# Kernel optimization log

Hardware: AMD Instinct MI355X
Metric: run time of the kernel (lower is better)

The kernel has to match this reference:

```python
import jax, jax.numpy as jnp
import numpy as np

B, S, HIDDEN = 2, 2048, 2048
HQ, HKV, D = 16, 4, 128
EPS = 1e-6
SCALE = D ** -0.5


def _deinterleave(x):
    # [..., D] interleaved pairs -> [x0,x2,...,x1,x3,...] (half layout)
    *lead, d = x.shape
    return x.reshape(*lead, d // 2, 2).swapaxes(-1, -2).reshape(*lead, d)


def _interleave(x):
    # inverse of _deinterleave
    *lead, d = x.shape
    return x.reshape(*lead, 2, d // 2).swapaxes(-1, -2).reshape(*lead, d)


def _rotate_half(x):
    x1, x2 = jnp.split(x, 2, axis=-1)
    return jnp.concatenate([-x2, x1], axis=-1)


def _rmsnorm(x, w):
    var = jnp.mean(jnp.square(x), axis=-1, keepdims=True)
    return x * jax.lax.rsqrt(var + EPS) * w


def setup_inputs() -> dict:
    key = jax.random.key(0)
    k0, k1, k2, k3, k4 = jax.random.split(key, 5)
    hidden_states = jax.random.normal(k0, (B, S, HIDDEN), jnp.float32)
    cos = jax.random.uniform(k1, (S, D), jnp.float32, -1.0, 1.0)
    sin = jax.random.uniform(k2, (S, D), jnp.float32, -1.0, 1.0)
    qkv_w = jax.random.normal(k3, ((HQ + 2 * HKV) * D, HIDDEN), jnp.float32) * 0.02
    qk_norm_w = jnp.ones((D,), jnp.float32)
    o_w = jax.random.normal(k4, (HIDDEN, HQ * D), jnp.float32) * 0.02
    return {"hidden_states": hidden_states, "cos": cos, "sin": sin,
            "qkv_w": qkv_w, "qk_norm_w": qk_norm_w, "o_w": o_w}


def reference(hidden_states, cos, sin, qkv_w, qk_norm_w, o_w):
    b, s, _ = hidden_states.shape
    qkv = jnp.einsum('bsh,oh->bso', hidden_states, qkv_w)  # [B,S,(HQ+2HKV)*D]
    q = qkv[..., : HQ * D].reshape(b, s, HQ, D)
    k = qkv[..., HQ * D:(HQ + HKV) * D].reshape(b, s, HKV, D)
    v = qkv[..., (HQ + HKV) * D:].reshape(b, s, HKV, D)

    # interleaved-layout RoPE: deinterleave -> rotate-half RoPE -> re-interleave
    q, k = _deinterleave(q), _deinterleave(k)
    cs = cos[None, :, None, :]
    sn = sin[None, :, None, :]
    q = q * cs + _rotate_half(q) * sn
    k = k * cs + _rotate_half(k) * sn
    q, k = _interleave(q), _interleave(k)

    # QK RMSNorm (shared weight over head_dim)
    q = _rmsnorm(q, qk_norm_w)
    k = _rmsnorm(k, qk_norm_w)

    # causal GQA attention
    g = HQ // HKV
    qg = q.reshape(b, s, HKV, g, D)
    scores = jnp.einsum('bshgd,bthd->bhgst', qg, k) * SCALE  # [B,HKV,g,S,S]
    causal = jnp.tril(jnp.ones((s, s), bool))
    scores = jnp.where(causal, scores, jnp.finfo(scores.dtype).min)
    probs = jax.nn.softmax(scores, axis=-1)
    attn = jnp.einsum('bhgst,bthd->bshgd', probs, v).reshape(b, s, HQ * D)

    return jnp.einsum('bsd,od->bso', attn, o_w)
```

## Files before the change

kernel.cpp:

```cpp
#include <hip/hip_runtime.h>
#include <hip/hip_bf16.h>

typedef __bf16 bf16_t;
typedef bf16_t bf16x8 __attribute__((ext_vector_type(8)));
typedef float f32x4 __attribute__((ext_vector_type(4)));
typedef float f32x16 __attribute__((ext_vector_type(16)));
typedef unsigned short u16;
typedef unsigned int u32;

#define B_    2
#define S_    2048
#define HID   2048
#define NQKV  3072
#define HQ_   16
#define HKV_  4
#define D_    128
#define QSCALE_ 0.12751879526600565f

__device__ __forceinline__ u16 f2b(float f) {
    __hip_bfloat16 h = __float2bfloat16(f);
    return *reinterpret_cast<u16*>(&h);
}
__device__ __forceinline__ float b2f(u32 u) {
    u32 v = u << 16;
    float f;
    __builtin_memcpy(&f, &v, 4);
    return f;
}

__global__ __launch_bounds__(256) void cvt3_f32_bf16(const float* __restrict__ i0, u16* __restrict__ o0, int n0,
                                                     const float* __restrict__ i1, u16* __restrict__ o1, int n1,
                                                     const float* __restrict__ i2, u16* __restrict__ o2, int n2) {
    int i = blockIdx.x * 256 + threadIdx.x;
    const float* src; u16* dst; int idx;
    if (i < n0)           { src = i0; dst = o0; idx = i; }
    else if (i < n0 + n1) { src = i1; dst = o1; idx = i - n0; }
    else if (i < n0 + n1 + n2) { src = i2; dst = o2; idx = i - n0 - n1; }
    else return;
    float4 v = reinterpret_cast<const float4*>(src)[idx];
    ushort4 o;
    o.x = f2b(v.x); o.y = f2b(v.y); o.z = f2b(v.z); o.w = f2b(v.w);
    reinterpret_cast<ushort4*>(dst)[idx] = o;
}

template<bool BF16OUT>
__global__ __launch_bounds__(256, 2) void gemm128sq(const u16* __restrict__ A,
                                                    const u16* __restrict__ Bm,
                                                    void* __restrict__ Cv,
                                                    int M, int N, int K) {
    __shared__ __align__(16) char smem[2][32768];

    const int tid  = threadIdx.x;
    const int lane = tid & 63;
    const int wid  = tid >> 6;
    const int wr = wid >> 1, wc = wid & 1;
    const int l31 = lane & 31, hi = lane >> 5;
    const int swz = (l31 & 7) << 4;

    const int m0 = blockIdx.x * 128, n0 = blockIdx.y * 128;

    const int stRow = tid >> 3;
    const int stColE = ((((tid & 7) * 16) ^ ((stRow & 7) << 4)) >> 1);
    const u16* aBase = A  + (size_t)(m0 + stRow) * K + stColE;
    const u16* bBase = Bm + (size_t)(n0 + stRow) * K + stColE;

    auto glds = [&](const u16* g, u16* l) {
        __builtin_amdgcn_global_load_lds(
            (const __attribute__((address_space(1))) void*)g,
            (__attribute__((address_space(3))) void*)l, 16, 0, 0);
    };
    auto stage = [&](int buf, int k0) {
        u16* ad = (u16*)smem[buf] + tid * 8;
        u16* bd = ad + 8192;
        #pragma unroll
        for (int p = 0; p < 4; ++p)
            glds(aBase + (size_t)(p * 32) * K + k0, ad + p * 2048);
        #pragma unroll
        for (int p = 0; p < 4; ++p)
            glds(bBase + (size_t)(p * 32) * K + k0, bd + p * 2048);
    };

    f32x16 acc[2][2] = {};
    const int KT = K >> 6;

    stage(0, 0);

    for (int t = 0; t < KT; ++t) {
        const int cur = t & 1;
        if (t + 1 < KT) {
            stage(cur ^ 1, (t + 1) << 6);
            asm volatile("s_waitcnt vmcnt(8)" ::: "memory");
        } else {
            asm volatile("s_waitcnt vmcnt(0)" ::: "memory");
        }
        __builtin_amdgcn_s_barrier();

        const char* aT = smem[cur];
        const char* bT = aT + 16384;

        #pragma unroll
        for (int ks = 0; ks < 4; ++ks) {
            const int kb = (ks * 32 + hi * 16) ^ swz;
            bf16x8 af0 = *(const bf16x8*)(aT + (wr * 64 +      l31) * 128 + kb);
            bf16x8 af1 = *(const bf16x8*)(aT + (wr * 64 + 32 + l31) * 128 + kb);
            bf16x8 bf0 = *(const bf16x8*)(bT + (wc * 64 +      l31) * 128 + kb);
            bf16x8 bf1 = *(const bf16x8*)(bT + (wc * 64 + 32 + l31) * 128 + kb);
            __builtin_amdgcn_s_setprio(1);
            acc[0][0] = __builtin_amdgcn_mfma_f32_32x32x16_bf16(af0, bf0, acc[0][0], 0, 0, 0);
            acc[0][1] = __builtin_amdgcn_mfma_f32_32x32x16_bf16(af0, bf1, acc[0][1], 0, 0, 0);
            acc[1][0] = __builtin_amdgcn_mfma_f32_32x32x16_bf16(af1, bf0, acc[1][0], 0, 0, 0);
            acc[1][1] = __builtin_amdgcn_mfma_f32_32x32x16_bf16(af1, bf1, acc[1][1], 0, 0, 0);
            __builtin_amdgcn_s_setprio(0);
        }
        __builtin_amdgcn_s_barrier();
    }

    #pragma unroll
    for (int mb = 0; mb < 2; ++mb)
        #pragma unroll
        for (int nb = 0; nb < 2; ++nb) {
            const int n = n0 + wc * 64 + nb * 32 + l31;
            #pragma unroll
            for (int r = 0; r < 16; ++r) {
                int m = m0 + wr * 64 + mb * 32 + (r & 3) + 8 * (r >> 2) + 4 * hi;
                if (BF16OUT)
                    ((u16*)Cv)[(size_t)m * N + n] = f2b(acc[mb][nb][r]);
                else
                    ((float*)Cv)[(size_t)m * N + n] = acc[mb][nb][r];
            }
        }
}

__global__ __launch_bounds__(256) void rope_norm_split(const u16* __restrict__ qkvb,
                                                       const float* __restrict__ cosb,
                                                       const float* __restrict__ sinb,
                                                       const float* __restrict__ nw,
                                                       u16* __restrict__ qb,
                                                       u16* __restrict__ kb,
                                                       u16* __restrict__ vb) {
    const int row  = blockIdx.x;
    const int b    = row >> 11;
    const int s    = row & 2047;
    const int wave = threadIdx.x >> 6;
    const int lane = threadIdx.x & 63;
    const u16* base = qkvb + (size_t)row * NQKV;

    const float c0 = cosb[s * 128 + lane];
    const float c1 = cosb[s * 128 + 64 + lane];
    const float s0 = sinb[s * 128 + lane];
    const float s1 = sinb[s * 128 + 64 + lane];
    const float w0 = nw[2 * lane];
    const float w1 = nw[2 * lane + 1];

    for (int h = wave; h < HQ_ + HKV_; h += 4) {
        u32 xw = *(const u32*)(base + h * 128 + 2 * lane);
        float x0 = b2f(xw & 0xffffu), x1 = b2f(xw >> 16);
        float y0 = x0 * c0 - x1 * s0;
        float y1 = x1 * c1 + x0 * s1;
        float ss = y0 * y0 + y1 * y1;
        #pragma unroll
        for (int off = 32; off; off >>= 1) ss += __shfl_xor(ss, off);
        float r = rsqrtf(ss * (1.0f / 128.0f) + 1e-6f);
        float o0 = y0 * r * w0, o1 = y1 * r * w1;
        if (h < HQ_) {
            u32 pack = (u32)f2b(o0 * QSCALE_) | ((u32)f2b(o1 * QSCALE_) << 16);
            *(u32*)(qb + ((size_t)(b * HQ_ + h) * S_ + s) * D_ + 2 * lane) = pack;
        } else {
            u32 pack = (u32)f2b(o0) | ((u32)f2b(o1) << 16);
            *(u32*)(kb + ((size_t)(b * HKV_ + (h - HQ_)) * S_ + s) * D_ + 2 * lane) = pack;
        }
    }
    {
        int h = wave;
        u32 xw = *(const u32*)(base + (HQ_ + HKV_) * 128 + h * 128 + 2 * lane);
        *(u32*)(vb + ((size_t)(b * HKV_ + h) * S_ + s) * D_ + 2 * lane) = xw;
    }
}

__global__ __launch_bounds__(256) void transpose_v(const u16* __restrict__ vb,
                                                   u16* __restrict__ vtb) {
    __shared__ u16 t[64][72];
    const int s0 = blockIdx.x * 64, d0 = blockIdx.y * 64, bh = blockIdx.z;
    const u16* src = vb  + (size_t)bh * S_ * D_;
    u16*       dst = vtb + (size_t)bh * D_ * S_;
    const int tid = threadIdx.x;

    {
        int r = tid >> 3, c8 = (tid & 7) * 8;
        #pragma unroll
        for (int p = 0; p < 2; p++) {
            int rr = r + p * 32;
            *(uint4*)&t[rr][c8] = *(const uint4*)(src + (size_t)(s0 + rr) * D_ + d0 + c8);
        }
    }
    __syncthreads();
    {
        int dd = tid & 63;
        int sb = (tid >> 6) * 8;
        #pragma unroll
        for (int p = 0; p < 2; p++) {
            int ss8 = sb + p * 32;
            union { u16 u[8]; uint4 v; } pk;
            #pragma unroll
            for (int j = 0; j < 8; j++) pk.u[j] = t[ss8 + j][dd];
            *(uint4*)(dst + (size_t)(d0 + dd) * S_ + s0 + ss8) = pk.v;
        }
    }
}

__global__ __launch_bounds__(256, 2) void attn_fwd3(const u16* __restrict__ qb,
                                                    const u16* __restrict__ kb,
                                                    const u16* __restrict__ vtb,
                                                    u16* __restrict__ attn) {
    __shared__ __align__(16) u16 Ks[2][64 * 128];
    __shared__ __align__(16) u16 Vs[2][64 * 128];

    const int bh  = blockIdx.y;
    const int qt  = (bh < 16) ? (15 - (int)blockIdx.x) : (int)blockIdx.x;
    const int b   = bh >> 4, hq = bh & 15, hkv = hq >> 2;
    const int tid = threadIdx.x;
    const int wave = tid >> 6, lane = tid & 63;
    const int l31 = lane & 31, hi = lane >> 5;
    const int swzK = (l31 & 15) << 4;
    const int swzO = (l31 & 7) << 4;

    const u16* Q  = qb  + (size_t)(b * HQ_  + hq ) * S_ * D_;
    const u16* Kp = kb  + (size_t)(b * HKV_ + hkv) * S_ * D_;
    const u16* Vt = vtb + (size_t)(b * HKV_ + hkv) * D_ * S_;
    const int q0w = qt * 128 + wave * 32;
    const int qg  = q0w + l31;

    int kSrc[4], vSrc[4], cLds[4];
    #pragma unroll
    for (int p = 0; p < 4; p++) {
        int c = tid + p * 256;
        int kr = c >> 4;
        int kc = ((c & 15) * 16) ^ ((kr & 15) << 4);
        kSrc[p] = kr * D_ + (kc >> 1);
        int vr = c >> 4;
        int raw = (c & 15) ^ (vr & 15);
        int vd = 2 * vr + (raw >> 3);
        vSrc[p] = vd * S_ + (raw & 7) * 8;
        cLds[p] = c * 16;
    }

    auto STAGE = [&](int buf, int kv0s) {
        const u16* kbase = Kp + (size_t)kv0s * D_;
        const u16* vbase = Vt + kv0s;
        #pragma unroll
        for (int p = 0; p < 4; p++)
            __builtin_amdgcn_global_load_lds(
                (const __attribute__((address_space(1))) void*)(kbase + kSrc[p]),
                (__attribute__((address_space(3))) void*)((char*)Ks[buf] + cLds[p]), 16, 0, 0);
        #pragma unroll
        for (int p = 0; p < 4; p++)
            __builtin_amdgcn_global_load_lds(
                (const __attribute__((address_space(1))) void*)(vbase + vSrc[p]),
                (__attribute__((address_space(3))) void*)((char*)Vs[buf] + cLds[p]), 16, 0, 0);
    };

    bf16x8 qf[8];
    #pragma unroll
    for (int ds = 0; ds < 8; ds++)
        qf[ds] = *(const bf16x8*)(Q + (size_t)qg * D_ + ds * 16 + hi * 8);

    float m_run = -1e30f, l_run = 0.f;
    f32x16 oacc[4] = {};

    const int nkt = 2 * qt + 2;
    STAGE(0, 0);

    for (int kt = 0; kt < nkt; kt++) {
        const int cur = kt & 1;
        const int kv0 = kt * 64;
        if (kt + 1 < nkt) {
            STAGE(cur ^ 1, kv0 + 64);
            asm volatile("s_waitcnt vmcnt(8)" ::: "memory");
        } else {
            asm volatile("s_waitcnt vmcnt(0)" ::: "memory");
        }
        __builtin_amdgcn_s_barrier();

        const char* ksb = (const char*)Ks[cur];
        const char* vsb = (const char*)Vs[cur];
        const char* rb0 = ksb + l31 * 256;
        const char* rb1 = rb0 + 32 * 256;
        bf16x8 kA[8], kB[8];
        #pragma unroll
        for (int ds = 0; ds < 8; ds++) kA[ds] = *(const bf16x8*)(rb0 + ((ds * 32 + hi * 16) ^ swzK));
        #pragma unroll
        for (int ds = 0; ds < 8; ds++) kB[ds] = *(const bf16x8*)(rb1 + ((ds * 32 + hi * 16) ^ swzK));

        f32x16 s0a = {}, s0b = {}, s1a = {}, s1b = {};
        __builtin_amdgcn_s_setprio(1);
        #pragma unroll
        for (int ds = 0; ds < 4; ds++) {
            s0a = __builtin_amdgcn_mfma_f32_32x32x16_bf16(kA[ds],     qf[ds],     s0a, 0, 0, 0);
            s0b = __builtin_amdgcn_mfma_f32_32x32x16_bf16(kA[ds + 4], qf[ds + 4], s0b, 0, 0, 0);
            s1a = __builtin_amdgcn_mfma_f32_32x32x16_bf16(kB[ds],     qf[ds],     s1a, 0, 0, 0);
            s1b = __builtin_amdgcn_mfma_f32_32x32x16_bf16(kB[ds + 4], qf[ds + 4], s1b, 0, 0, 0);
        }
        __builtin_amdgcn_s_setprio(0);
        f32x16 sc[2];
        sc[0] = s0a + s0b;
        sc[1] = s1a + s1b;

        bf16x8 vf[4][4];
        {
            const int vrow = (l31 >> 1);
            const int vswz = vrow << 4;
            const int dlo  = (l31 & 1) << 7;
            #pragma unroll
            for (int ks = 0; ks < 4; ks++)
                #pragma unroll
                for (int d4 = 0; d4 < 4; d4++)
                    vf[ks][d4] = *(const bf16x8*)(vsb + (d4 * 16 + vrow) * 256
                                                      + ((dlo | (ks * 32 + hi * 16)) ^ vswz));
        }
        __builtin_amdgcn_s_barrier();

        if (kv0 + 63 > q0w) {
            #pragma unroll
            for (int blk = 0; blk < 2; blk++)
                #pragma unroll
                for (int r = 0; r < 16; r++) {
                    int kvg = kv0 + blk * 32 + (r & 3) + 8 * (r >> 2) + 4 * hi;
                    if (kvg > qg) sc[blk][r] = -1e30f;
                }
        }

        float t16[16];
        #pragma unroll
        for (int r = 0; r < 16; r++) t16[r] = fmaxf(sc[0][r], sc[1][r]);
        #pragma unroll
        for (int r = 0; r < 8; r++) t16[r] = fmaxf(t16[r], t16[r + 8]);
        #pragma unroll
        for (int r = 0; r < 4; r++) t16[r] = fmaxf(t16[r], t16[r + 4]);
        float mt = fmaxf(fmaxf(t16[0], t16[1]), fmaxf(t16[2], t16[3]));
        mt = fmaxf(mt, __shfl_xor(mt, 32));

        bool noDefer = !__all(mt <= m_run + 8.0f);
        float mnew = m_run;
        if (noDefer) {
            mnew = fmaxf(m_run, mt);
            float alpha = __builtin_amdgcn_exp2f(m_run - mnew);
            l_run *= alpha;
            #pragma unroll
            for (int d4 = 0; d4 < 4; d4++)
                #pragma unroll
                for (int r = 0; r < 16; r++) oacc[d4][r] *= alpha;
            m_run = mnew;
        }

        float la = 0.f;
        u32 pk0[8], pk1[8];
        #pragma unroll
        for (int g = 0; g < 4; g++)
            #pragma unroll
            for (int e = 0; e < 2; e++) {
                float a0 = __builtin_amdgcn_exp2f(sc[0][g * 4 + 2 * e]     - mnew);
                float b0 = __builtin_amdgcn_exp2f(sc[0][g * 4 + 2 * e + 1] - mnew);
                float a1 = __builtin_amdgcn_exp2f(sc[1][g * 4 + 2 * e]     - mnew);
                float b1 = __builtin_amdgcn_exp2f(sc[1][g * 4 + 2 * e + 1] - mnew);
                la += (a0 + b0) + (a1 + b1);
                pk0[g * 2 + e] = (u32)f2b(a0) | ((u32)f2b(b0) << 16);
                pk1[g * 2 + e] = (u32)f2b(a1) | ((u32)f2b(b1) << 16);
            }
        la += __shfl_xor(la, 32);
        l_run += la;

        u32 qk0[8], qk1[8];
        #pragma unroll
        for (int i = 0; i < 8; i++) {
            qk0[i] = __shfl_xor(pk0[i], 32);
            qk1[i] = __shfl_xor(pk1[i], 32);
        }

        #pragma unroll
        for (int ks = 0; ks < 4; ks++) {
            const int i0 = (ks & 1) * 4;
            union { u32 w[4]; bf16x8 v; } pfv;
            if (ks & 2) {
                pfv.w[0] = hi ? qk1[i0 + 2] : pk1[i0 + 0];
                pfv.w[1] = hi ? qk1[i0 + 3] : pk1[i0 + 1];
                pfv.w[2] = hi ? pk1[i0 + 2] : qk1[i0 + 0];
                pfv.w[3] = hi ? pk1[i0 + 3] : qk1[i0 + 1];
            } else {
                pfv.w[0] = hi ? qk0[i0 + 2] : pk0[i0 + 0];
                pfv.w[1] = hi ? qk0[i0 + 3] : pk0[i0 + 1];
                pfv.w[2] = hi ? pk0[i0 + 2] : qk0[i0 + 0];
                pfv.w[3] = hi ? pk0[i0 + 3] : qk0[i0 + 1];
            }
            __builtin_amdgcn_s_setprio(1);
            #pragma unroll
            for (int d4 = 0; d4 < 4; d4++)
                oacc[d4] = __builtin_amdgcn_mfma_f32_32x32x16_bf16(vf[ks][d4], pfv.v, oacc[d4], 0, 0, 0);
            __builtin_amdgcn_s_setprio(0);
        }
    }

    const float inv = 1.0f / l_run;
    u16* sl = (u16*)Ks + wave * (32 * 128);
    #pragma unroll
    for (int d4 = 0; d4 < 4; d4++)
        #pragma unroll
        for (int rp = 0; rp < 8; rp++) {
            int dbyte = d4 * 64 + 16 * (rp >> 1) + 8 * hi + 4 * (rp & 1);
            u32 w = (u32)f2b(oacc[d4][rp * 2] * inv)
                  | ((u32)f2b(oacc[d4][rp * 2 + 1] * inv) << 16);
            *(u32*)((char*)sl + l31 * 256 + (dbyte ^ swzO)) = w;
        }
    #pragma unroll
    for (int j = 0; j < 8; j++) {
        int c = lane + j * 64;
        int qL = c >> 4, dc = c & 15;
        uint4 v = *(uint4*)((char*)sl + qL * 256 + ((dc * 16) ^ ((qL & 7) << 4)));
        int qrow = qt * 128 + wave * 32 + qL;
        *(uint4*)(attn + (size_t)(b * S_ + qrow) * (HQ_ * D_) + hq * D_ + dc * 8) = v;
    }
}

extern "C" void kernel_launch(void* const* d_in, const int* in_sizes, int n_in,
                              void* d_out, int out_size, void* d_ws, size_t ws_size,
                              hipStream_t stream) {
    const float* hidden = (const float*)d_in[0];
    const float* cosb   = (const float*)d_in[1];
    const float* sinb   = (const float*)d_in[2];
    const float* qkvw   = (const float*)d_in[3];
    const float* nw     = (const float*)d_in[4];
    const float* ow     = (const float*)d_in[5];
    float* out = (float*)d_out;

    const size_t M  = (size_t)B_ * S_;
    char* ws = (char*)d_ws;
    size_t off = 0;
    u16*   hb    = (u16*)(ws + off); off += M * HID * 2;
    u16*   wqkvb = (u16*)(ws + off); off += (size_t)NQKV * HID * 2;
    u16*   wob   = (u16*)(ws + off); off += (size_t)HID * (HQ_ * D_) * 2;
    u16*   qkvb  = (u16*)(ws + off); off += M * NQKV * 2;
    u16*   qb2   = (u16*)(ws + off); off += (size_t)B_ * HQ_  * S_ * D_ * 2;
    u16*   kb2   = (u16*)(ws + off); off += (size_t)B_ * HKV_ * S_ * D_ * 2;
    u16*   vb2   = (u16*)(ws + off); off += (size_t)B_ * HKV_ * S_ * D_ * 2;
    u16*   vtb   = (u16*)(ws + off); off += (size_t)B_ * HKV_ * S_ * D_ * 2;
    u16*   attn  = hb;

    {
        int n0 = (int)(M * HID / 4);
        int n1 = NQKV * HID / 4;
        int n2 = HID * (HQ_ * D_) / 4;
        int nt = n0 + n1 + n2;
        cvt3_f32_bf16<<<(nt + 255) / 256, 256, 0, stream>>>(hidden, hb, n0,
                                                            qkvw, wqkvb, n1,
                                                            ow, wob, n2);
    }

    gemm128sq<true><<<dim3(M / 128, NQKV / 128), 256, 0, stream>>>(
        hb, wqkvb, qkvb, (int)M, NQKV, HID);

    rope_norm_split<<<(int)M, 256, 0, stream>>>(qkvb, cosb, sinb, nw, qb2, kb2, vb2);

    transpose_v<<<dim3(S_ / 64, D_ / 64, B_ * HKV_), 256, 0, stream>>>(vb2, vtb);

    attn_fwd3<<<dim3(16, B_ * HQ_), 256, 0, stream>>>(qb2, kb2, vtb, attn);

    gemm128sq<false><<<dim3(M / 128, HID / 128), 256, 0, stream>>>(
        attn, wob, out, (int)M, HID, HQ_ * D_);
}
```

Baseline: 218.3 us.

## Load K tiles straight into registers with double buffering, bypassing LDS

K tiles are no longer staged through shared memory. Each wave now reads its K rows from global memory directly into two ping-pong register sets, prefetching the next tile while the current one is used. The main loop is unrolled by two to swap those buffers. Only V is still staged in LDS, and the output epilogue reuses the V buffer with an added barrier. This removes the K LDS writes and reads and halves LDS use, but every wave now fetches the full K tile from global or L2, and the extra 128 VGPRs of K buffers raise the risk of spills at two blocks per CU.

Measured after the change: 384.6 us. 76.2% more time.

```diff
diff --git a/kernel.cpp b/kernel.cpp
--- a/kernel.cpp
+++ b/kernel.cpp
@@ -212,7 +212,6 @@
                                                     const u16* __restrict__ kb,
                                                     const u16* __restrict__ vtb,
                                                     u16* __restrict__ attn) {
-    __shared__ __align__(16) u16 Ks[2][64 * 128];
     __shared__ __align__(16) u16 Vs[2][64 * 128];
 
     const int bh  = blockIdx.y;
@@ -221,7 +220,6 @@
     const int tid = threadIdx.x;
     const int wave = tid >> 6, lane = tid & 63;
     const int l31 = lane & 31, hi = lane >> 5;
-    const int swzK = (l31 & 15) << 4;
     const int swzO = (l31 & 7) << 4;
 
     const u16* Q  = qb  + (size_t)(b * HQ_  + hq ) * S_ * D_;
@@ -230,13 +228,10 @@
     const int q0w = qt * 128 + wave * 32;
     const int qg  = q0w + l31;
 
-    int kSrc[4], vSrc[4], cLds[4];
+    int vSrc[4], cLds[4];
     #pragma unroll
     for (int p = 0; p < 4; p++) {
         int c = tid + p * 256;
-        int kr = c >> 4;
-        int kc = ((c & 15) * 16) ^ ((kr & 15) << 4);
-        kSrc[p] = kr * D_ + (kc >> 1);
         int vr = c >> 4;
         int raw = (c & 15) ^ (vr & 15);
         int vd = 2 * vr + (raw >> 3);
@@ -244,14 +239,8 @@
         cLds[p] = c * 16;
     }
 
-    auto STAGE = [&](int buf, int kv0s) {
-        const u16* kbase = Kp + (size_t)kv0s * D_;
+    auto STAGE_V = [&](int buf, int kv0s) {
         const u16* vbase = Vt + kv0s;
-        #pragma unroll
-        for (int p = 0; p < 4; p++)
-            __builtin_amdgcn_global_load_lds(
-                (const __attribute__((address_space(1))) void*)(kbase + kSrc[p]),
-                (__attribute__((address_space(3))) void*)((char*)Ks[buf] + cLds[p]), 16, 0, 0);
         #pragma unroll
         for (int p = 0; p < 4; p++)
             __builtin_amdgcn_global_load_lds(
@@ -259,6 +248,9 @@
                 (__attribute__((address_space(3))) void*)((char*)Vs[buf] + cLds[p]), 16, 0, 0);
     };
 
+    const int rowOffA = l31 * D_ + hi * 8;
+    const int rowOffB = (32 + l31) * D_ + hi * 8;
+
     bf16x8 qf[8];
     #pragma unroll
     for (int ds = 0; ds < 8; ds++)
@@ -268,43 +260,54 @@
     f32x16 oacc[4] = {};
 
     const int nkt = 2 * qt + 2;
-    STAGE(0, 0);
-
-    for (int kt = 0; kt < nkt; kt++) {
+
+    bf16x8 kA0[8], kB0[8], kA1[8], kB1[8];
+
+    #pragma unroll
+    for (int ds = 0; ds < 8; ds++) {
+        kA0[ds] = *(const bf16x8*)(Kp + rowOffA + ds * 16);
+        kB0[ds] = *(const bf16x8*)(Kp + rowOffB + ds * 16);
+    }
+    STAGE_V(0, 0);
+
+    auto BODY = [&](int kt, bf16x8 (&cA)[8], bf16x8 (&cB)[8],
+                    bf16x8 (&nA)[8], bf16x8 (&nB)[8]) {
+        const int kv0 = kt * 64;
         const int cur = kt & 1;
-        const int kv0 = kt * 64;
-        if (kt + 1 < nkt) {
-            STAGE(cur ^ 1, kv0 + 64);
-            asm volatile("s_waitcnt vmcnt(8)" ::: "memory");
+        const bool pf = (kt + 1 < nkt);
+
+        if (pf) {
+            STAGE_V(cur ^ 1, kv0 + 64);
+            asm volatile("s_waitcnt vmcnt(4)" ::: "memory");
         } else {
             asm volatile("s_waitcnt vmcnt(0)" ::: "memory");
         }
         __builtin_amdgcn_s_barrier();
 
-        const char* ksb = (const char*)Ks[cur];
-        const char* vsb = (const char*)Vs[cur];
-        const char* rb0 = ksb + l31 * 256;
-        const char* rb1 = rb0 + 32 * 256;
-        bf16x8 kA[8], kB[8];
-        #pragma unroll
-        for (int ds = 0; ds < 8; ds++) kA[ds] = *(const bf16x8*)(rb0 + ((ds * 32 + hi * 16) ^ swzK));
-        #pragma unroll
-        for (int ds = 0; ds < 8; ds++) kB[ds] = *(const bf16x8*)(rb1 + ((ds * 32 + hi * 16) ^ swzK));
-
         f32x16 s0a = {}, s0b = {}, s1a = {}, s1b = {};
         __builtin_amdgcn_s_setprio(1);
         #pragma unroll
         for (int ds = 0; ds < 4; ds++) {
-            s0a = __builtin_amdgcn_mfma_f32_32x32x16_bf16(kA[ds],     qf[ds],     s0a, 0, 0, 0);
-            s0b = __builtin_amdgcn_mfma_f32_32x32x16_bf16(kA[ds + 4], qf[ds + 4], s0b, 0, 0, 0);
-            s1a = __builtin_amdgcn_mfma_f32_32x32x16_bf16(kB[ds],     qf[ds],     s1a, 0, 0, 0);
-            s1b = __builtin_amdgcn_mfma_f32_32x32x16_bf16(kB[ds + 4], qf[ds + 4], s1b, 0, 0, 0);
+            s0a = __builtin_amdgcn_mfma_f32_32x32x16_bf16(cA[ds],     qf[ds],     s0a, 0, 0, 0);
+            s0b = __builtin_amdgcn_mfma_f32_32x32x16_bf16(cA[ds + 4], qf[ds + 4], s0b, 0, 0, 0);
+            s1a = __builtin_amdgcn_mfma_f32_32x32x16_bf16(cB[ds],     qf[ds],     s1a, 0, 0, 0);
+            s1b = __builtin_amdgcn_mfma_f32_32x32x16_bf16(cB[ds + 4], qf[ds + 4], s1b, 0, 0, 0);
         }
         __builtin_amdgcn_s_setprio(0);
         f32x16 sc[2];
         sc[0] = s0a + s0b;
         sc[1] = s1a + s1b;
 
+        if (pf) {
+            const u16* kN = Kp + (size_t)(kv0 + 64) * D_;
+            #pragma unroll
+            for (int ds = 0; ds < 8; ds++) {
+                nA[ds] = *(const bf16x8*)(kN + rowOffA + ds * 16);
+                nB[ds] = *(const bf16x8*)(kN + rowOffB + ds * 16);
+            }
+        }
+
+        const char* vsb = (const char*)Vs[cur];
         bf16x8 vf[4][4];
         {
             const int vrow = (l31 >> 1);
@@ -397,10 +400,15 @@
                 oacc[d4] = __builtin_amdgcn_mfma_f32_32x32x16_bf16(vf[ks][d4], pfv.v, oacc[d4], 0, 0, 0);
             __builtin_amdgcn_s_setprio(0);
         }
+    };
+
+    for (int kt2 = 0; kt2 < nkt; kt2 += 2) {
+        BODY(kt2,     kA0, kB0, kA1, kB1);
+        BODY(kt2 + 1, kA1, kB1, kA0, kB0);
     }
 
     const float inv = 1.0f / l_run;
-    u16* sl = (u16*)Ks + wave * (32 * 128);
+    u16* sl = (u16*)Vs + wave * (32 * 128);
     #pragma unroll
     for (int d4 = 0; d4 < 4; d4++)
         #pragma unroll
@@ -410,6 +418,7 @@
                   | ((u32)f2b(oacc[d4][rp * 2 + 1] * inv) << 16);
             *(u32*)((char*)sl + l31 * 256 + (dbyte ^ swzO)) = w;
         }
+    __builtin_amdgcn_s_barrier();
     #pragma unroll
     for (int j = 0; j < 8; j++) {
         int c = lane + j * 64;
```
